# Kernel optimization log

Hardware: AMD Instinct MI355X
Metric: run time of the kernel (lower is better)

Reference implementation:

```python
import jax, jax.numpy as jnp
import numpy as np

D = 64      # features
H = 512     # hidden width of the vector field MLP
B = 4096    # batch
NSTEPS = 17 # t_span grid points -> 16 RK4 steps


def setup_inputs() -> dict:
    key = jax.random.key(0)
    ks = jax.random.split(key, 8)
    x = jax.random.normal(ks[0], (B, D), dtype=jnp.float32)
    t_span = jnp.linspace(0.0, 1.0, NSTEPS, dtype=jnp.float32)
    # MLP vector field params: concat(x, t) -> H -> H -> D, tanh activations
    W1 = jax.random.normal(ks[1], (D + 1, H), dtype=jnp.float32) / np.sqrt(D + 1)
    b1 = jnp.zeros((H,), dtype=jnp.float32)
    W2 = jax.random.normal(ks[2], (H, H), dtype=jnp.float32) / np.sqrt(H)
    b2 = jnp.zeros((H,), dtype=jnp.float32)
    W3 = jax.random.normal(ks[3], (H, D), dtype=jnp.float32) / np.sqrt(H)
    b3 = jnp.zeros((D,), dtype=jnp.float32)
    return {"x": x, "t_span": t_span, "W1": W1, "b1": b1,
            "W2": W2, "b2": b2, "W3": W3, "b3": b3}


def _vf_single(params, t, xi):
    # xi: (D,) single sample; t: scalar
    W1, b1, W2, b2, W3, b3 = params
    h = jnp.concatenate([xi, jnp.reshape(t, (1,)).astype(xi.dtype)])
    h = jnp.tanh(h @ W1 + b1)
    h = jnp.tanh(h @ W2 + b2)
    return h @ W3 + b3


def _vf(params, t, x):
    # x: (B, D) batched evaluation
    W1, b1, W2, b2, W3, b3 = params
    tb = jnp.full((x.shape[0], 1), t, dtype=x.dtype)
    h = jnp.tanh(jnp.concatenate([x, tb], axis=-1) @ W1 + b1)
    h = jnp.tanh(h @ W2 + b2)
    return h @ W3 + b3


def _divergence_exact(params, t, x):
    # Exact trace of Jacobian df/dx per sample via forward-mode (D JVPs).
    f = lambda xi: _vf_single(params, t, xi)
    J = jax.vmap(jax.jacfwd(f))(x)          # [B, D, D]
    return jnp.trace(J, axis1=-2, axis2=-1)  # [B]


def _aug_dynamics(params, t, state):
    # state: [B, D+1] = [x, log_det]; d(log_det)/dt = -trace(df/dx)
    x = state[:, :-1]
    dx = _vf(params, t, x)
    tr = _divergence_exact(params, t, x)
    return jnp.concatenate([dx, -tr[:, None]], axis=-1)


def _odeint_rk4(params, state0, t_span):
    ts = t_span[:-1]
    dts = jnp.diff(t_span)

    def step(s, td):
        t, dt = td
        k1 = _aug_dynamics(params, t, s)
        k2 = _aug_dynamics(params, t + dt * 0.5, s + dt * 0.5 * k1)
        k3 = _aug_dynamics(params, t + dt * 0.5, s + dt * 0.5 * k2)
        k4 = _aug_dynamics(params, t + dt, s + dt * k3)
        return s + (dt / 6.0) * (k1 + 2.0 * k2 + 2.0 * k3 + k4), None

    s, _ = jax.lax.scan(step, state0, (ts, dts))
    return s


def reference(x, t_span, W1, b1, W2, b2, W3, b3):
    params = (W1, b1, W2, b2, W3, b3)
    log_det0 = jnp.zeros((x.shape[0], 1), dtype=x.dtype)
    state0 = jnp.concatenate([x, log_det0], axis=-1)  # [B, D+1]
    state_final = _odeint_rk4(params, state0, t_span)
    z = state_final[:, :-1]
    log_det = state_final[:, -1]
    return z, log_det
```

## Files before the change

kernel.cpp:

```cpp
#include <hip/hip_runtime.h>


#define NSTEP 16
#define TSAMP 16

typedef short v8s __attribute__((ext_vector_type(8)));
typedef float v4f __attribute__((ext_vector_type(4)));

__device__ __forceinline__ short bf16r(float x) {
    unsigned u = __builtin_bit_cast(unsigned, x);
    u = u + 0x7FFFu + ((u >> 16) & 1u);
    return (short)(u >> 16);
}
__device__ __forceinline__ float tanh_fast(float x) {
    float e = __expf(2.0f * x);
    return 1.0f - 2.0f / (e + 1.0f);
}

__global__ __launch_bounds__(256) void cnf_prep(
    const float* __restrict__ W1, const float* __restrict__ W2,
    const float* __restrict__ W3, short* __restrict__ ws)
{
  int t = blockIdx.x * 256 + threadIdx.x;
  short* W2s = ws;
  short* Cs  = ws + 262144;
  short* W1s = ws + 524288;
  short* W3s = ws + 557056;
  if (t < 32768) {
    int l = t & 63;
    int tk = t >> 6;
    int ks = tk & 15, ntile = tk >> 4;
    int n = ntile * 16 + (l & 15);
    int kbase = ks * 32 + (l >> 4) * 8;
    v8s wv, cv;
#pragma unroll
    for (int e = 0; e < 8; ++e) {
      int k = kbase + e;
      float w2 = W2[k * 512 + n];
      float g = 0.0f;
      for (int i = 0; i < 64; ++i)
        g += W1[i * 512 + k] * W3[n * 64 + i];
      wv[e] = bf16r(w2);
      cv[e] = bf16r(w2 * g);
    }
    ((v8s*)W2s)[t] = wv;
    ((v8s*)Cs)[t]  = cv;
  } else if (t < 36864) {
    int u = t - 32768;
    int l = u & 63, tk = u >> 6;
    int ks = tk & 1, ntile = tk >> 1;
    int n = ntile * 16 + (l & 15);
    int kbase = ks * 32 + (l >> 4) * 8;
    v8s wv;
#pragma unroll
    for (int e = 0; e < 8; ++e)
      wv[e] = bf16r(W1[(kbase + e) * 512 + n]);
    ((v8s*)W1s)[u] = wv;
  } else if (t < 40960) {
    int u = t - 36864;
    int l = u & 63, tk = u >> 6;
    int ks = tk & 15, ntile = tk >> 4;
    int n = ntile * 16 + (l & 15);
    int kbase = ks * 32 + (l >> 4) * 8;
    v8s wv;
#pragma unroll
    for (int e = 0; e < 8; ++e)
      wv[e] = bf16r(W3[(kbase + e) * 64 + n]);
    ((v8s*)W3s)[u] = wv;
  }
}

__global__ __launch_bounds__(512) void cnf_main(
    const float* __restrict__ x_in, const float* __restrict__ t_span,
    const float* __restrict__ W1, const float* __restrict__ b1,
    const float* __restrict__ b2, const float* __restrict__ b3,
    const short* __restrict__ ws, float* __restrict__ out)
{
  const int tid = threadIdx.x;
  const int lane = tid & 63;
  const int w = tid >> 6;
  const int l15 = lane & 15;
  const int l16 = lane >> 4;
  const int b0 = blockIdx.x * TSAMP;

  const short* W2s = ws;
  const short* Cs  = ws + 262144;
  const short* W1s = ws + 524288;
  const short* W3s = ws + 557056;

  __shared__ __align__(16) short xbf[16 * 64];
  __shared__ __align__(16) short h1bf[16 * 512];
  __shared__ __align__(16) short h2bf[16 * 512];
  __shared__ __align__(16) float x0s[16 * 64];
  __shared__ __align__(16) float xas[16 * 64];
  __shared__ __align__(16) char sdx[16 * 512 * 2];
  __shared__ float trs[16];
  __shared__ float ld0s[16];
  __shared__ float ldas[16];

  short* s1bf = (short*)sdx;
  float (*dxp)[16 * 64] = (float (*)[16 * 64])sdx;

  for (int i = tid; i < 1024; i += 512) {
    int row = i >> 6, col = i & 63;
    float v = x_in[(size_t)(b0 + row) * 64 + col];
    x0s[i] = v;
    int byte = row * 128 + col * 2;
    byte ^= (row & 7) << 4;
    *(short*)((char*)xbf + byte) = bf16r(v);
  }
  if (tid < 16) { ld0s[tid] = 0.0f; trs[tid] = 0.0f; }
  __syncthreads();

  for (int step = 0; step < NSTEP; ++step) {
    float t0 = t_span[step];
    float dt = t_span[step + 1] - t0;
#pragma unroll 1
    for (int st = 0; st < 4; ++st) {
      float tc = (st == 0) ? t0 : ((st == 3) ? (t0 + dt) : (t0 + 0.5f * dt));

#pragma unroll
      for (int nt = 0; nt < 4; ++nt) {
        int ng = w * 4 + nt;
        v4f acc = {0.f, 0.f, 0.f, 0.f};
#pragma unroll
        for (int ks = 0; ks < 2; ++ks) {
          int byte = l15 * 128 + ks * 64 + l16 * 16;
          byte ^= (l15 & 7) << 4;
          v8s a = *(const v8s*)((const char*)xbf + byte);
          v8s b = ((const v8s*)W1s)[(ng * 2 + ks) * 64 + lane];
          acc = __builtin_amdgcn_mfma_f32_16x16x32_bf16(a, b, acc, 0, 0, 0);
        }
        int col = ng * 16 + l15;
        float bias = b1[col] + tc * W1[64 * 512 + col];
#pragma unroll
        for (int r = 0; r < 4; ++r) {
          float h = tanh_fast(acc[r] + bias);
          int row = l16 * 4 + r;
          int byte = row * 1024 + col * 2;
          byte ^= (row & 7) << 4;
          *(short*)((char*)h1bf + byte) = bf16r(h);
          *(short*)((char*)s1bf + byte) = bf16r(1.0f - h * h);
        }
      }
      __syncthreads();

      {
        v4f acc2[4] = {};
        v4f accv[4] = {};
        for (int ks = 0; ks < 16; ++ks) {
          int byte = l15 * 1024 + ks * 64 + l16 * 16;
          byte ^= (l15 & 7) << 4;
          v8s a1 = *(const v8s*)((const char*)h1bf + byte);
          v8s as = *(const v8s*)((const char*)s1bf + byte);
#pragma unroll
          for (int nt = 0; nt < 4; ++nt) {
            int ng = w * 4 + nt;
            v8s bw = ((const v8s*)W2s)[(ng * 16 + ks) * 64 + lane];
            v8s bc = ((const v8s*)Cs)[(ng * 16 + ks) * 64 + lane];
            acc2[nt] = __builtin_amdgcn_mfma_f32_16x16x32_bf16(a1, bw, acc2[nt], 0, 0, 0);
            accv[nt] = __builtin_amdgcn_mfma_f32_16x16x32_bf16(as, bc, accv[nt], 0, 0, 0);
          }
        }
        float trp[4] = {0.f, 0.f, 0.f, 0.f};
#pragma unroll
        for (int nt = 0; nt < 4; ++nt) {
          int col = w * 64 + nt * 16 + l15;
          float bias = b2[col];
#pragma unroll
          for (int r = 0; r < 4; ++r) {
            float h = tanh_fast(acc2[nt][r] + bias);
            float s2 = 1.0f - h * h;
            int row = l16 * 4 + r;
            int byte = row * 1024 + col * 2;
            byte ^= (row & 7) << 4;
            *(short*)((char*)h2bf + byte) = bf16r(h);
            trp[r] += accv[nt][r] * s2;
          }
        }
#pragma unroll
        for (int m = 1; m < 16; m <<= 1) {
#pragma unroll
          for (int r = 0; r < 4; ++r)
            trp[r] += __shfl_xor(trp[r], m, 64);
        }
        if (l15 == 0) {
#pragma unroll
          for (int r = 0; r < 4; ++r)
            atomicAdd(&trs[l16 * 4 + r], trp[r]);
        }
      }
      __syncthreads();

      if (w < 4) {
        v4f acc3[4] = {};
#pragma unroll
        for (int kk = 0; kk < 4; ++kk) {
          int ks = w * 4 + kk;
          int byte = l15 * 1024 + ks * 64 + l16 * 16;
          byte ^= (l15 & 7) << 4;
          v8s a = *(const v8s*)((const char*)h2bf + byte);
#pragma unroll
          for (int nt = 0; nt < 4; ++nt) {
            v8s b = ((const v8s*)W3s)[(nt * 16 + ks) * 64 + lane];
            acc3[nt] = __builtin_amdgcn_mfma_f32_16x16x32_bf16(a, b, acc3[nt], 0, 0, 0);
          }
        }
#pragma unroll
        for (int nt = 0; nt < 4; ++nt)
#pragma unroll
          for (int r = 0; r < 4; ++r)
            dxp[w][(l16 * 4 + r) * 64 + nt * 16 + l15] = acc3[nt][r];
      }
      __syncthreads();

      for (int i = tid; i < 1024; i += 512) {
        int row = i >> 6, col = i & 63;
        float dxv = b3[col];
#pragma unroll
        for (int ww = 0; ww < 4; ++ww) dxv += dxp[ww][i];
        float x0v = x0s[i];
        float xsn;
        if (st == 0)      { xas[i] = x0v + (dt * (1.0f/6.0f)) * dxv; xsn = x0v + 0.5f * dt * dxv; }
        else if (st == 1) { xas[i] += (dt * (1.0f/3.0f)) * dxv;      xsn = x0v + 0.5f * dt * dxv; }
        else if (st == 2) { xas[i] += (dt * (1.0f/3.0f)) * dxv;      xsn = x0v + dt * dxv; }
        else              { float nx = xas[i] + (dt * (1.0f/6.0f)) * dxv; x0s[i] = nx; xsn = nx; }
        int byte = row * 128 + col * 2;
        byte ^= (row & 7) << 4;
        *(short*)((char*)xbf + byte) = bf16r(xsn);
      }
      if (tid < 16) {
        float kld = -trs[tid];
        trs[tid] = 0.0f;
        if (st == 0)      ldas[tid] = ld0s[tid] + (dt * (1.0f/6.0f)) * kld;
        else if (st == 3) ld0s[tid] = ldas[tid] + (dt * (1.0f/6.0f)) * kld;
        else              ldas[tid] += (dt * (1.0f/3.0f)) * kld;
      }
      __syncthreads();
    }
  }

  for (int i = tid; i < 1024; i += 512)
    out[(size_t)(b0 + (i >> 6)) * 64 + (i & 63)] = x0s[i];
  if (tid < 16)
    out[262144 + b0 + tid] = ld0s[tid];
}

extern "C" void kernel_launch(void* const* d_in, const int* in_sizes, int n_in,
                              void* d_out, int out_size, void* d_ws, size_t ws_size,
                              hipStream_t stream) {
  const float* x  = (const float*)d_in[0];
  const float* ts = (const float*)d_in[1];
  const float* W1 = (const float*)d_in[2];
  const float* b1 = (const float*)d_in[3];
  const float* W2 = (const float*)d_in[4];
  const float* b2 = (const float*)d_in[5];
  const float* W3 = (const float*)d_in[6];
  const float* b3 = (const float*)d_in[7];
  short* ws = (short*)d_ws;
  float* outp = (float*)d_out;

  hipLaunchKernelGGL(cnf_prep, dim3(160), dim3(256), 0, stream, W1, W2, W3, ws);
  hipLaunchKernelGGL(cnf_main, dim3(256), dim3(512), 0, stream,
                     x, ts, W1, b1, b2, b3, (const short*)ws, outp);
}
```

Baseline: 837.5 us.

## Process 32 samples per block to reuse weight fragments across two M tiles

Doubles the per-block sample tile from 16 to 32 rows, so each weight fragment loaded from global memory (W1, W2, C, W3) feeds two MFMA row tiles instead of one. This halves the weight traffic per sample in the dominant second-layer loop, which streams W2 and C from L2 every substep. The third-layer GEMM now uses all 8 waves, split as 2 row tiles by 4 k-slices. In exchange the grid shrinks to 128 blocks on a 256-CU device, leaving half the CUs idle, and LDS use and register pressure roughly double.

```diff
diff --git a/kernel.cpp b/kernel.cpp
--- a/kernel.cpp
+++ b/kernel.cpp
@@ -2,7 +2,7 @@
 
 
 #define NSTEP 16
-#define TSAMP 16
+#define TSAMP 32
 
 typedef short v8s __attribute__((ext_vector_type(8)));
 typedef float v4f __attribute__((ext_vector_type(4)));
@@ -88,28 +88,27 @@
   const short* W1s = ws + 524288;
   const short* W3s = ws + 557056;
 
-  __shared__ __align__(16) short xbf[16 * 64];
-  __shared__ __align__(16) short h1bf[16 * 512];
-  __shared__ __align__(16) short h2bf[16 * 512];
-  __shared__ __align__(16) float x0s[16 * 64];
-  __shared__ __align__(16) float xas[16 * 64];
-  __shared__ __align__(16) char sdx[16 * 512 * 2];
-  __shared__ float trs[16];
-  __shared__ float ld0s[16];
-  __shared__ float ldas[16];
+  __shared__ __align__(16) short xbf[32 * 64];
+  __shared__ __align__(16) short h1bf[32 * 512];
+  __shared__ __align__(16) short h2bf[32 * 512];
+  __shared__ __align__(16) float x0s[32 * 64];
+  __shared__ __align__(16) float xas[32 * 64];
+  __shared__ __align__(16) char sdx[32 * 512 * 2];
+  __shared__ float trs[32];
+  __shared__ float ld0s[32];
+  __shared__ float ldas[32];
 
   short* s1bf = (short*)sdx;
-  float (*dxp)[16 * 64] = (float (*)[16 * 64])sdx;
-
-  for (int i = tid; i < 1024; i += 512) {
+  float (*dxp)[32 * 64] = (float (*)[32 * 64])sdx;
+
+  for (int i = tid; i < 2048; i += 512) {
     int row = i >> 6, col = i & 63;
     float v = x_in[(size_t)(b0 + row) * 64 + col];
     x0s[i] = v;
-    int byte = row * 128 + col * 2;
-    byte ^= (row & 7) << 4;
+    int byte = (row * 128 + col * 2) ^ ((row & 7) << 4);
     *(short*)((char*)xbf + byte) = bf16r(v);
   }
-  if (tid < 16) { ld0s[tid] = 0.0f; trs[tid] = 0.0f; }
+  if (tid < 32) { ld0s[tid] = 0.0f; trs[tid] = 0.0f; }
   __syncthreads();
 
   for (int step = 0; step < NSTEP; ++step) {
@@ -119,86 +118,112 @@
     for (int st = 0; st < 4; ++st) {
       float tc = (st == 0) ? t0 : ((st == 3) ? (t0 + dt) : (t0 + 0.5f * dt));
 
-#pragma unroll
-      for (int nt = 0; nt < 4; ++nt) {
-        int ng = w * 4 + nt;
-        v4f acc = {0.f, 0.f, 0.f, 0.f};
-#pragma unroll
-        for (int ks = 0; ks < 2; ++ks) {
-          int byte = l15 * 128 + ks * 64 + l16 * 16;
-          byte ^= (l15 & 7) << 4;
-          v8s a = *(const v8s*)((const char*)xbf + byte);
-          v8s b = ((const v8s*)W1s)[(ng * 2 + ks) * 64 + lane];
-          acc = __builtin_amdgcn_mfma_f32_16x16x32_bf16(a, b, acc, 0, 0, 0);
-        }
-        int col = ng * 16 + l15;
-        float bias = b1[col] + tc * W1[64 * 512 + col];
-#pragma unroll
-        for (int r = 0; r < 4; ++r) {
-          float h = tanh_fast(acc[r] + bias);
-          int row = l16 * 4 + r;
-          int byte = row * 1024 + col * 2;
-          byte ^= (row & 7) << 4;
-          *(short*)((char*)h1bf + byte) = bf16r(h);
-          *(short*)((char*)s1bf + byte) = bf16r(1.0f - h * h);
-        }
-      }
-      __syncthreads();
-
       {
-        v4f acc2[4] = {};
-        v4f accv[4] = {};
+        v8s ax[2][2];
+#pragma unroll
+        for (int m = 0; m < 2; ++m)
+#pragma unroll
+          for (int ks = 0; ks < 2; ++ks) {
+            int byte = ((m * 16 + l15) * 128 + ks * 64 + l16 * 16)
+                       ^ ((l15 & 7) << 4);
+            ax[m][ks] = *(const v8s*)((const char*)xbf + byte);
+          }
+#pragma unroll
+        for (int nt = 0; nt < 4; ++nt) {
+          int ng = w * 4 + nt;
+          v4f acc0 = {0.f, 0.f, 0.f, 0.f};
+          v4f acc1 = {0.f, 0.f, 0.f, 0.f};
+#pragma unroll
+          for (int ks = 0; ks < 2; ++ks) {
+            v8s b = ((const v8s*)W1s)[(ng * 2 + ks) * 64 + lane];
+            acc0 = __builtin_amdgcn_mfma_f32_16x16x32_bf16(ax[0][ks], b, acc0, 0, 0, 0);
+            acc1 = __builtin_amdgcn_mfma_f32_16x16x32_bf16(ax[1][ks], b, acc1, 0, 0, 0);
+          }
+          int col = ng * 16 + l15;
+          float bias = b1[col] + tc * W1[64 * 512 + col];
+#pragma unroll
+          for (int m = 0; m < 2; ++m) {
+            v4f accm = (m == 0) ? acc0 : acc1;
+#pragma unroll
+            for (int r = 0; r < 4; ++r) {
+              float h = tanh_fast(accm[r] + bias);
+              int row = m * 16 + l16 * 4 + r;
+              int byte = (row * 1024 + col * 2) ^ ((row & 7) << 4);
+              *(short*)((char*)h1bf + byte) = bf16r(h);
+              *(short*)((char*)s1bf + byte) = bf16r(1.0f - h * h);
+            }
+          }
+        }
+      }
+      __syncthreads();
+
+      {
+        v4f acc2[4][2] = {};
+        v4f accv[4][2] = {};
         for (int ks = 0; ks < 16; ++ks) {
-          int byte = l15 * 1024 + ks * 64 + l16 * 16;
-          byte ^= (l15 & 7) << 4;
-          v8s a1 = *(const v8s*)((const char*)h1bf + byte);
-          v8s as = *(const v8s*)((const char*)s1bf + byte);
+          v8s a1[2], as[2];
+#pragma unroll
+          for (int m = 0; m < 2; ++m) {
+            int byte = ((m * 16 + l15) * 1024 + ks * 64 + l16 * 16)
+                       ^ ((l15 & 7) << 4);
+            a1[m] = *(const v8s*)((const char*)h1bf + byte);
+            as[m] = *(const v8s*)((const char*)s1bf + byte);
+          }
 #pragma unroll
           for (int nt = 0; nt < 4; ++nt) {
             int ng = w * 4 + nt;
             v8s bw = ((const v8s*)W2s)[(ng * 16 + ks) * 64 + lane];
             v8s bc = ((const v8s*)Cs)[(ng * 16 + ks) * 64 + lane];
-            acc2[nt] = __builtin_amdgcn_mfma_f32_16x16x32_bf16(a1, bw, acc2[nt], 0, 0, 0);
-            accv[nt] = __builtin_amdgcn_mfma_f32_16x16x32_bf16(as, bc, accv[nt], 0, 0, 0);
-          }
-        }
-        float trp[4] = {0.f, 0.f, 0.f, 0.f};
+#pragma unroll
+            for (int m = 0; m < 2; ++m) {
+              acc2[nt][m] = __builtin_amdgcn_mfma_f32_16x16x32_bf16(a1[m], bw, acc2[nt][m], 0, 0, 0);
+              accv[nt][m] = __builtin_amdgcn_mfma_f32_16x16x32_bf16(as[m], bc, accv[nt][m], 0, 0, 0);
+            }
+          }
+        }
+        float trp[2][4] = {};
 #pragma unroll
         for (int nt = 0; nt < 4; ++nt) {
           int col = w * 64 + nt * 16 + l15;
           float bias = b2[col];
 #pragma unroll
-          for (int r = 0; r < 4; ++r) {
-            float h = tanh_fast(acc2[nt][r] + bias);
-            float s2 = 1.0f - h * h;
-            int row = l16 * 4 + r;
-            int byte = row * 1024 + col * 2;
-            byte ^= (row & 7) << 4;
-            *(short*)((char*)h2bf + byte) = bf16r(h);
-            trp[r] += accv[nt][r] * s2;
-          }
-        }
-#pragma unroll
-        for (int m = 1; m < 16; m <<= 1) {
-#pragma unroll
-          for (int r = 0; r < 4; ++r)
-            trp[r] += __shfl_xor(trp[r], m, 64);
+          for (int m = 0; m < 2; ++m)
+#pragma unroll
+            for (int r = 0; r < 4; ++r) {
+              float h = tanh_fast(acc2[nt][m][r] + bias);
+              float s2 = 1.0f - h * h;
+              int row = m * 16 + l16 * 4 + r;
+              int byte = (row * 1024 + col * 2) ^ ((row & 7) << 4);
+              *(short*)((char*)h2bf + byte) = bf16r(h);
+              trp[m][r] += accv[nt][m][r] * s2;
+            }
+        }
+#pragma unroll
+        for (int msk = 1; msk < 16; msk <<= 1) {
+#pragma unroll
+          for (int m = 0; m < 2; ++m)
+#pragma unroll
+            for (int r = 0; r < 4; ++r)
+              trp[m][r] += __shfl_xor(trp[m][r], msk, 64);
         }
         if (l15 == 0) {
 #pragma unroll
-          for (int r = 0; r < 4; ++r)
-            atomicAdd(&trs[l16 * 4 + r], trp[r]);
-        }
-      }
-      __syncthreads();
-
-      if (w < 4) {
+          for (int m = 0; m < 2; ++m)
+#pragma unroll
+            for (int r = 0; r < 4; ++r)
+              atomicAdd(&trs[m * 16 + l16 * 4 + r], trp[m][r]);
+        }
+      }
+      __syncthreads();
+
+      {
+        int m3 = w >> 2, k4 = w & 3;
         v4f acc3[4] = {};
 #pragma unroll
         for (int kk = 0; kk < 4; ++kk) {
-          int ks = w * 4 + kk;
-          int byte = l15 * 1024 + ks * 64 + l16 * 16;
-          byte ^= (l15 & 7) << 4;
+          int ks = k4 * 4 + kk;
+          int byte = ((m3 * 16 + l15) * 1024 + ks * 64 + l16 * 16)
+                     ^ ((l15 & 7) << 4);
           v8s a = *(const v8s*)((const char*)h2bf + byte);
 #pragma unroll
           for (int nt = 0; nt < 4; ++nt) {
@@ -210,11 +235,11 @@
         for (int nt = 0; nt < 4; ++nt)
 #pragma unroll
           for (int r = 0; r < 4; ++r)
-            dxp[w][(l16 * 4 + r) * 64 + nt * 16 + l15] = acc3[nt][r];
-      }
-      __syncthreads();
-
-      for (int i = tid; i < 1024; i += 512) {
+            dxp[k4][(m3 * 16 + l16 * 4 + r) * 64 + nt * 16 + l15] = acc3[nt][r];
+      }
+      __syncthreads();
+
+      for (int i = tid; i < 2048; i += 512) {
         int row = i >> 6, col = i & 63;
         float dxv = b3[col];
 #pragma unroll
@@ -225,11 +250,10 @@
         else if (st == 1) { xas[i] += (dt * (1.0f/3.0f)) * dxv;      xsn = x0v + 0.5f * dt * dxv; }
         else if (st == 2) { xas[i] += (dt * (1.0f/3.0f)) * dxv;      xsn = x0v + dt * dxv; }
         else              { float nx = xas[i] + (dt * (1.0f/6.0f)) * dxv; x0s[i] = nx; xsn = nx; }
-        int byte = row * 128 + col * 2;
-        byte ^= (row & 7) << 4;
+        int byte = (row * 128 + col * 2) ^ ((row & 7) << 4);
         *(short*)((char*)xbf + byte) = bf16r(xsn);
       }
-      if (tid < 16) {
+      if (tid < 32) {
         float kld = -trs[tid];
         trs[tid] = 0.0f;
         if (st == 0)      ldas[tid] = ld0s[tid] + (dt * (1.0f/6.0f)) * kld;
@@ -240,9 +264,9 @@
     }
   }
 
-  for (int i = tid; i < 1024; i += 512)
+  for (int i = tid; i < 2048; i += 512)
     out[(size_t)(b0 + (i >> 6)) * 64 + (i & 63)] = x0s[i];
-  if (tid < 16)
+  if (tid < 32)
     out[262144 + b0 + tid] = ld0s[tid];
 }
 
@@ -261,6 +285,6 @@
   float* outp = (float*)d_out;
 
   hipLaunchKernelGGL(cnf_prep, dim3(160), dim3(256), 0, stream, W1, W2, W3, ws);
-  hipLaunchKernelGGL(cnf_main, dim3(256), dim3(512), 0, stream,
+  hipLaunchKernelGGL(cnf_main, dim3(128), dim3(512), 0, stream,
                      x, ts, W1, b1, b2, b3, (const short*)ws, outp);
 }
```

New measurement: 1.381 ms. +64.9%, slower.

## Split layer-2 GEMM and trace GEMM across separate wave groups

Applied to the files above, without the earlier changes.

Waves 0-3 now compute the full H1·W2 product (8 column tiles each) and write h2. Waves 4-7 compute the s1·C divergence product on their own and hold the result in registers. The trace reduction moves into the layer-3 phase, where waves 4-7 read back the bf16 h2 to form the tanh derivative while waves 0-3 run the W3 GEMM. This is meant to overlap the trace epilogue with layer 3 and to give each wave a single operand stream, at the cost of more accumulator registers per wave and a trace computed from bf16-rounded h2.

```diff
diff --git a/kernel.cpp b/kernel.cpp
--- a/kernel.cpp
+++ b/kernel.cpp
@@ -11,6 +11,10 @@
     unsigned u = __builtin_bit_cast(unsigned, x);
     u = u + 0x7FFFu + ((u >> 16) & 1u);
     return (short)(u >> 16);
+}
+__device__ __forceinline__ float bf2f(short s) {
+    unsigned u = ((unsigned)(unsigned short)s) << 16;
+    return __builtin_bit_cast(float, u);
 }
 __device__ __forceinline__ float tanh_fast(float x) {
     float e = __expf(2.0f * x);
@@ -145,49 +149,40 @@
       }
       __syncthreads();
 
-      {
-        v4f acc2[4] = {};
-        v4f accv[4] = {};
+      v4f accv[8] = {};
+      if (w < 4) {
+        v4f acc2[8] = {};
         for (int ks = 0; ks < 16; ++ks) {
-          int byte = l15 * 1024 + ks * 64 + l16 * 16;
-          byte ^= (l15 & 7) << 4;
+          int byte = (l15 * 1024 + ks * 64 + l16 * 16) ^ ((l15 & 7) << 4);
           v8s a1 = *(const v8s*)((const char*)h1bf + byte);
-          v8s as = *(const v8s*)((const char*)s1bf + byte);
-#pragma unroll
-          for (int nt = 0; nt < 4; ++nt) {
-            int ng = w * 4 + nt;
-            v8s bw = ((const v8s*)W2s)[(ng * 16 + ks) * 64 + lane];
-            v8s bc = ((const v8s*)Cs)[(ng * 16 + ks) * 64 + lane];
+#pragma unroll
+          for (int nt = 0; nt < 8; ++nt) {
+            v8s bw = ((const v8s*)W2s)[((w * 8 + nt) * 16 + ks) * 64 + lane];
             acc2[nt] = __builtin_amdgcn_mfma_f32_16x16x32_bf16(a1, bw, acc2[nt], 0, 0, 0);
-            accv[nt] = __builtin_amdgcn_mfma_f32_16x16x32_bf16(as, bc, accv[nt], 0, 0, 0);
-          }
-        }
-        float trp[4] = {0.f, 0.f, 0.f, 0.f};
-#pragma unroll
-        for (int nt = 0; nt < 4; ++nt) {
-          int col = w * 64 + nt * 16 + l15;
+          }
+        }
+#pragma unroll
+        for (int nt = 0; nt < 8; ++nt) {
+          int col = (w * 8 + nt) * 16 + l15;
           float bias = b2[col];
 #pragma unroll
           for (int r = 0; r < 4; ++r) {
             float h = tanh_fast(acc2[nt][r] + bias);
-            float s2 = 1.0f - h * h;
             int row = l16 * 4 + r;
-            int byte = row * 1024 + col * 2;
-            byte ^= (row & 7) << 4;
+            int byte = (row * 1024 + col * 2) ^ ((row & 7) << 4);
             *(short*)((char*)h2bf + byte) = bf16r(h);
-            trp[r] += accv[nt][r] * s2;
-          }
-        }
-#pragma unroll
-        for (int m = 1; m < 16; m <<= 1) {
-#pragma unroll
-          for (int r = 0; r < 4; ++r)
-            trp[r] += __shfl_xor(trp[r], m, 64);
-        }
-        if (l15 == 0) {
-#pragma unroll
-          for (int r = 0; r < 4; ++r)
-            atomicAdd(&trs[l16 * 4 + r], trp[r]);
+          }
+        }
+      } else {
+        int w4 = w - 4;
+        for (int ks = 0; ks < 16; ++ks) {
+          int byte = (l15 * 1024 + ks * 64 + l16 * 16) ^ ((l15 & 7) << 4);
+          v8s as = *(const v8s*)((const char*)s1bf + byte);
+#pragma unroll
+          for (int nt = 0; nt < 8; ++nt) {
+            v8s bc = ((const v8s*)Cs)[((w4 * 8 + nt) * 16 + ks) * 64 + lane];
+            accv[nt] = __builtin_amdgcn_mfma_f32_16x16x32_bf16(as, bc, accv[nt], 0, 0, 0);
+          }
         }
       }
       __syncthreads();
@@ -211,6 +206,31 @@
 #pragma unroll
           for (int r = 0; r < 4; ++r)
             dxp[w][(l16 * 4 + r) * 64 + nt * 16 + l15] = acc3[nt][r];
+      } else {
+        int w4 = w - 4;
+        float trp[4] = {0.f, 0.f, 0.f, 0.f};
+#pragma unroll
+        for (int nt = 0; nt < 8; ++nt) {
+          int col = (w4 * 8 + nt) * 16 + l15;
+#pragma unroll
+          for (int r = 0; r < 4; ++r) {
+            int row = l16 * 4 + r;
+            int byte = (row * 1024 + col * 2) ^ ((row & 7) << 4);
+            float h = bf2f(*(const short*)((const char*)h2bf + byte));
+            trp[r] += accv[nt][r] * (1.0f - h * h);
+          }
+        }
+#pragma unroll
+        for (int m = 1; m < 16; m <<= 1) {
+#pragma unroll
+          for (int r = 0; r < 4; ++r)
+            trp[r] += __shfl_xor(trp[r], m, 64);
+        }
+        if (l15 == 0) {
+#pragma unroll
+          for (int r = 0; r < 4; ++r)
+            atomicAdd(&trs[l16 * 4 + r], trp[r]);
+        }
       }
       __syncthreads();
 
```

New measurement: 1.410 ms. +68.4%, slower.
